# Performance work log

Measured on AMD Instinct MI355X. Metric: run time of the kernel, lower is better.

The kernel has to match this reference:

```python
import jax, jax.numpy as jnp
import numpy as np

B, V, DEMB, H, LAT, L = 16384, 64, 128, 512, 128, 2
PAD, BOS, EOS = 0, 1, 2


def setup_inputs() -> dict:
    key = jax.random.key(0)
    ks = jax.random.split(key, 12)
    s = 0.05  # small init so softmax logits stay well-scaled
    z = jax.random.normal(ks[0], (B, LAT), jnp.float32)
    E = jax.random.normal(ks[1], (V, DEMB), jnp.float32) * s
    E = E.at[PAD].set(0.0)  # padding_idx row is zero
    W_l2h = jax.random.normal(ks[2], (H, LAT), jnp.float32) * s
    b_l2h = jnp.zeros((H,), jnp.float32)
    W_ih0 = jax.random.normal(ks[3], (4 * H, DEMB), jnp.float32) * s
    W_hh0 = jax.random.normal(ks[4], (4 * H, H), jnp.float32) * s
    b_ih0 = jnp.zeros((4 * H,), jnp.float32)
    b_hh0 = jnp.zeros((4 * H,), jnp.float32)
    W_ih1 = jax.random.normal(ks[5], (4 * H, H), jnp.float32) * s
    W_hh1 = jax.random.normal(ks[6], (4 * H, H), jnp.float32) * s
    b_ih1 = jnp.zeros((4 * H,), jnp.float32)
    b_hh1 = jnp.zeros((4 * H,), jnp.float32)
    W_out = jax.random.normal(ks[7], (V, H), jnp.float32) * s
    b_out = jnp.zeros((V,), jnp.float32)
    return {"z": z, "E": E, "W_l2h": W_l2h, "b_l2h": b_l2h,
            "W_ih0": W_ih0, "W_hh0": W_hh0, "b_ih0": b_ih0, "b_hh0": b_hh0,
            "W_ih1": W_ih1, "W_hh1": W_hh1, "b_ih1": b_ih1, "b_hh1": b_hh1,
            "W_out": W_out, "b_out": b_out, "max_len": 100}


def _lstm_cell(x, h, c, Wih, Whh, bih, bhh):
    # torch LSTM gate order: i, f, g, o
    g = x @ Wih.T + bih + h @ Whh.T + bhh  # [B, 4H]
    i, f, gg, o = jnp.split(g, 4, axis=-1)
    c_new = jax.nn.sigmoid(f) * c + jax.nn.sigmoid(i) * jnp.tanh(gg)
    h_new = jax.nn.sigmoid(o) * jnp.tanh(c_new)
    return h_new, c_new


def reference(z, E, W_l2h, b_l2h, W_ih0, W_hh0, b_ih0, b_hh0,
              W_ih1, W_hh1, b_ih1, b_hh1, W_out, b_out, max_len):
    # initial states: c0 = latent2hidden(z) repeated over layers, h0 = 0
    c0 = z @ W_l2h.T + b_l2h                      # [B, H]
    c = jnp.stack([c0, c0])                       # [L, B, H]
    h = jnp.zeros_like(c)
    prev = jnp.full((B,), BOS, jnp.int32)
    is_end = jnp.zeros((B,), bool)
    keys = jax.random.split(jax.random.key(42), max_len)

    def step(carry, k):
        h, c, prev, is_end = carry
        x = E[prev]                               # [B, DEMB]
        h0, c0_ = _lstm_cell(x, h[0], c[0], W_ih0, W_hh0, b_ih0, b_hh0)
        h1, c1_ = _lstm_cell(h0, h[1], c[1], W_ih1, W_hh1, b_ih1, b_hh1)
        logits = h1 @ W_out.T + b_out             # [B, V]
        cur = jax.random.categorical(k, logits)   # same dist as Categorical(softmax(logits))
        is_end = is_end | (cur == EOS)            # mark eos; eos itself becomes pad
        cur = jnp.where(is_end, PAD, cur).astype(jnp.int32)
        return (jnp.stack([h0, h1]), jnp.stack([c0_, c1_]), cur, is_end), cur

    _, samples = jax.lax.scan(step, (h, c, prev, is_end), keys)  # [T, B]
    return samples.T                              # [B, T]
```

## Files before the change

kernel.cpp:

```cpp
#include <hip/hip_runtime.h>
#include <stdint.h>

#define B_    16384
#define V_    64
#define DEMB_ 128
#define H_    512
#define PAD_  0
#define BOS_  1
#define EOS_  2

__device__ __forceinline__ uint32_t rotl32(uint32_t v, int n) {
    return (v << n) | (v >> (32 - n));
}

__device__ __forceinline__ void tf2x32(uint32_t k0, uint32_t k1,
                                       uint32_t x0, uint32_t x1,
                                       uint32_t& o0, uint32_t& o1)
{
    const uint32_t k2 = k0 ^ k1 ^ 0x1BD11BDAu;
    x0 += k0; x1 += k1;
#define TFR(r) { x0 += x1; x1 = rotl32(x1, (r)); x1 ^= x0; }
    TFR(13) TFR(15) TFR(26) TFR(6)
    x0 += k1; x1 += k2 + 1u;
    TFR(17) TFR(29) TFR(16) TFR(24)
    x0 += k2; x1 += k0 + 2u;
    TFR(13) TFR(15) TFR(26) TFR(6)
    x0 += k0; x1 += k1 + 3u;
    TFR(17) TFR(29) TFR(16) TFR(24)
    x0 += k1; x1 += k2 + 4u;
    TFR(13) TFR(15) TFR(26) TFR(6)
    x0 += k2; x1 += k0 + 5u;
#undef TFR
    o0 = x0; o1 = x1;
}

__device__ __forceinline__ float sigm(float x) {
    return 1.0f / (1.0f + expf(-x));
}

__device__ __forceinline__ float4 ld4(const float* p) {
    return *reinterpret_cast<const float4*>(p);
}

__global__ __launch_bounds__(256)
void init_state(const float* __restrict__ z, const float* __restrict__ Wl,
                const float* __restrict__ bl,
                float* __restrict__ C0, float* __restrict__ C1,
                float* __restrict__ H0, float* __restrict__ H1)
{
    __shared__ __align__(16) float As[16][68];
    __shared__ __align__(16) float Bs[16][68];
    const int tid  = threadIdx.x;
    const int b0   = blockIdx.x * 64;
    const int j0   = blockIdx.y * 64;
    const int tx   = tid & 15, ty = tid >> 4;
    const int lrow = tid >> 2, lkq = tid & 3;

    float acc[4][4] = {};

    for (int kt = 0; kt < DEMB_ / 16; ++kt) {
        const int k0 = kt * 16;
        float4 av = ld4(z  + (size_t)(b0 + lrow) * DEMB_ + k0 + lkq * 4);
        float4 bv = ld4(Wl + (size_t)(j0 + lrow) * DEMB_ + k0 + lkq * 4);
        __syncthreads();
        As[lkq*4+0][lrow] = av.x; As[lkq*4+1][lrow] = av.y; As[lkq*4+2][lrow] = av.z; As[lkq*4+3][lrow] = av.w;
        Bs[lkq*4+0][lrow] = bv.x; Bs[lkq*4+1][lrow] = bv.y; Bs[lkq*4+2][lrow] = bv.z; Bs[lkq*4+3][lrow] = bv.w;
        __syncthreads();
#pragma unroll
        for (int kk = 0; kk < 16; ++kk) {
            float4 a4 = ld4(&As[kk][ty*4]);
            float4 b4 = ld4(&Bs[kk][tx*4]);
            float ar[4] = {a4.x, a4.y, a4.z, a4.w};
            float br[4] = {b4.x, b4.y, b4.z, b4.w};
#pragma unroll
            for (int r = 0; r < 4; ++r)
#pragma unroll
                for (int c = 0; c < 4; ++c)
                    acc[r][c] = fmaf(ar[r], br[c], acc[r][c]);
        }
    }

#pragma unroll
    for (int r = 0; r < 4; ++r) {
        const int b = b0 + ty * 4 + r;
        const int j = j0 + tx * 4;
        float4 cv = {acc[r][0] + bl[j+0], acc[r][1] + bl[j+1],
                     acc[r][2] + bl[j+2], acc[r][3] + bl[j+3]};
        float4 zz = {0.f, 0.f, 0.f, 0.f};
        *reinterpret_cast<float4*>(C0 + (size_t)b * H_ + j) = cv;
        *reinterpret_cast<float4*>(C1 + (size_t)b * H_ + j) = cv;
        *reinterpret_cast<float4*>(H0 + (size_t)b * H_ + j) = zz;
        *reinterpret_cast<float4*>(H1 + (size_t)b * H_ + j) = zz;
    }
}

__global__ __launch_bounds__(256)
void init_tokens(int* __restrict__ prevtok, int* __restrict__ isend)
{
    int i = blockIdx.x * 256 + threadIdx.x;
    if (i < B_) { prevtok[i] = BOS_; isend[i] = 0; }
}

template<int KX, bool GATHER>
__global__ __launch_bounds__(256, 2)
void lstm_layer(const float* __restrict__ Asrc,
                const int*   __restrict__ prevtok,
                const float* __restrict__ Hrec,
                const float* __restrict__ Wih,
                const float* __restrict__ Whh,
                const float* __restrict__ bih,
                const float* __restrict__ bhh,
                float* __restrict__ Cst,
                float* __restrict__ Hout)
{
    __shared__ __align__(16) float As[2][16][132];
    __shared__ __align__(16) float Bs[2][4][16][68];
    __shared__ int rowtok[128];

    const int tid  = threadIdx.x;
    const int bid  = blockIdx.x;
    const int b0   = (bid >> 3) * 128;
    const int j0   = (bid & 7) * 64;
    const int tx   = tid & 15;
    const int ty   = tid >> 4;
    const int srow = tid >> 1;
    const int sk   = (tid & 1) * 8;

    if (GATHER) {
        if (tid < 128) rowtok[tid] = prevtok[b0 + tid];
        __syncthreads();
    }

    const int grow0 = srow, grow1 = srow + 128;
    const int g0 = grow0 >> 6, u0 = grow0 & 63;
    const int g1 = grow1 >> 6, u1 = grow1 & 63;

    const float* arowA = GATHER ? (Asrc + (size_t)rowtok[srow] * DEMB_)
                                : (Asrc + (size_t)(b0 + srow) * KX);
    const float* arowH = Hrec + (size_t)(b0 + srow) * H_;
    const float* browA0 = Wih + (size_t)(g0 * H_ + j0 + u0) * KX;
    const float* browA1 = Wih + (size_t)(g1 * H_ + j0 + u1) * KX;
    const float* browH0 = Whh + (size_t)(g0 * H_ + j0 + u0) * H_;
    const float* browH1 = Whh + (size_t)(g1 * H_ + j0 + u1) * H_;

    const int NT = (KX + H_) / 16;

    float4 av[2], bv[4];

    auto load_tile = [&](int kt) {
        const int k0 = kt * 16;
        if (k0 < KX) {
            av[0] = ld4(arowA + k0 + sk);
            av[1] = ld4(arowA + k0 + sk + 4);
            bv[0] = ld4(browA0 + k0 + sk);
            bv[1] = ld4(browA0 + k0 + sk + 4);
            bv[2] = ld4(browA1 + k0 + sk);
            bv[3] = ld4(browA1 + k0 + sk + 4);
        } else {
            const int kh = k0 - KX;
            av[0] = ld4(arowH + kh + sk);
            av[1] = ld4(arowH + kh + sk + 4);
            bv[0] = ld4(browH0 + kh + sk);
            bv[1] = ld4(browH0 + kh + sk + 4);
            bv[2] = ld4(browH1 + kh + sk);
            bv[3] = ld4(browH1 + kh + sk + 4);
        }
    };

    auto write_tile = [&](int p) {
        float a0[4] = {av[0].x, av[0].y, av[0].z, av[0].w};
        float a1[4] = {av[1].x, av[1].y, av[1].z, av[1].w};
#pragma unroll
        for (int i = 0; i < 4; ++i) {
            As[p][sk + i][srow]     = a0[i];
            As[p][sk + 4 + i][srow] = a1[i];
        }
        float b0r[4] = {bv[0].x, bv[0].y, bv[0].z, bv[0].w};
        float b1r[4] = {bv[1].x, bv[1].y, bv[1].z, bv[1].w};
        float b2r[4] = {bv[2].x, bv[2].y, bv[2].z, bv[2].w};
        float b3r[4] = {bv[3].x, bv[3].y, bv[3].z, bv[3].w};
#pragma unroll
        for (int i = 0; i < 4; ++i) {
            Bs[p][g0][sk + i][u0]     = b0r[i];
            Bs[p][g0][sk + 4 + i][u0] = b1r[i];
            Bs[p][g1][sk + i][u1]     = b2r[i];
            Bs[p][g1][sk + 4 + i][u1] = b3r[i];
        }
    };

    load_tile(0);
    write_tile(0);
    load_tile(1);
    __syncthreads();

    float acc[4][8][4] = {};

    for (int kt = 0; kt < NT; ++kt) {
        const int cur = kt & 1;
        if (kt + 1 < NT) {
            write_tile(cur ^ 1);
            if (kt + 2 < NT) load_tile(kt + 2);
        }
#pragma unroll 4
        for (int kk = 0; kk < 16; ++kk) {
            float4 a40 = ld4(&As[cur][kk][ty*8]);
            float4 a41 = ld4(&As[cur][kk][ty*8+4]);
            float ar[8] = {a40.x, a40.y, a40.z, a40.w, a41.x, a41.y, a41.z, a41.w};
#pragma unroll
            for (int g = 0; g < 4; ++g) {
                float4 b4 = ld4(&Bs[cur][g][kk][tx*4]);
                float br[4] = {b4.x, b4.y, b4.z, b4.w};
#pragma unroll
                for (int r = 0; r < 8; ++r)
#pragma unroll
                    for (int c = 0; c < 4; ++c)
                        acc[g][r][c] = fmaf(ar[r], br[c], acc[g][r][c]);
            }
        }
        __syncthreads();
    }

    const int j = j0 + tx * 4;
    float4 bi0 = ld4(bih + 0*H_ + j), bi1 = ld4(bih + 1*H_ + j);
    float4 bi2 = ld4(bih + 2*H_ + j), bi3 = ld4(bih + 3*H_ + j);
    float4 bh0 = ld4(bhh + 0*H_ + j), bh1 = ld4(bhh + 1*H_ + j);
    float4 bh2 = ld4(bhh + 2*H_ + j), bh3 = ld4(bhh + 3*H_ + j);
    float bi[4][4] = {{bi0.x,bi0.y,bi0.z,bi0.w},{bi1.x,bi1.y,bi1.z,bi1.w},
                      {bi2.x,bi2.y,bi2.z,bi2.w},{bi3.x,bi3.y,bi3.z,bi3.w}};
    float bh[4][4] = {{bh0.x,bh0.y,bh0.z,bh0.w},{bh1.x,bh1.y,bh1.z,bh1.w},
                      {bh2.x,bh2.y,bh2.z,bh2.w},{bh3.x,bh3.y,bh3.z,bh3.w}};

#pragma unroll
    for (int r = 0; r < 8; ++r) {
        const int b = b0 + ty * 8 + r;
        float4 c4 = ld4(Cst + (size_t)b * H_ + j);
        float cold[4] = {c4.x, c4.y, c4.z, c4.w};
        float cn[4], hn[4];
#pragma unroll
        for (int c = 0; c < 4; ++c) {
            float gi = acc[0][r][c] + bi[0][c] + bh[0][c];
            float gf = acc[1][r][c] + bi[1][c] + bh[1][c];
            float gg = acc[2][r][c] + bi[2][c] + bh[2][c];
            float go = acc[3][r][c] + bi[3][c] + bh[3][c];
            float si = sigm(gi), sf = sigm(gf), so = sigm(go);
            float tg = tanhf(gg);
            float cc = __fadd_rn(__fmul_rn(sf, cold[c]), __fmul_rn(si, tg));
            cn[c] = cc;
            hn[c] = __fmul_rn(so, tanhf(cc));
        }
        float4 co = {cn[0], cn[1], cn[2], cn[3]};
        float4 ho = {hn[0], hn[1], hn[2], hn[3]};
        *reinterpret_cast<float4*>(Cst  + (size_t)b * H_ + j) = co;
        *reinterpret_cast<float4*>(Hout + (size_t)b * H_ + j) = ho;
    }
}

__global__ __launch_bounds__(256)
void sample_step(const float* __restrict__ H1src, const float* __restrict__ Wout,
                 const float* __restrict__ bout,
                 int* __restrict__ prevtok, int* __restrict__ isend,
                 int* __restrict__ out, int t, int T)
{
    __shared__ __align__(16) float As[16][68];
    __shared__ __align__(16) float Bs[16][68];
    __shared__ float LG[64][65];

    const int tid  = threadIdx.x;
    const int b0   = blockIdx.x * 64;
    const int tx   = tid & 15, ty = tid >> 4;
    const int lrow = tid >> 2, lkq = tid & 3;

    float acc[4][4] = {};

    for (int kt = 0; kt < H_ / 16; ++kt) {
        const int k0 = kt * 16;
        float4 av = ld4(H1src + (size_t)(b0 + lrow) * H_ + k0 + lkq * 4);
        float4 bv = ld4(Wout  + (size_t)lrow * H_ + k0 + lkq * 4);
        __syncthreads();
        As[lkq*4+0][lrow] = av.x; As[lkq*4+1][lrow] = av.y; As[lkq*4+2][lrow] = av.z; As[lkq*4+3][lrow] = av.w;
        Bs[lkq*4+0][lrow] = bv.x; Bs[lkq*4+1][lrow] = bv.y; Bs[lkq*4+2][lrow] = bv.z; Bs[lkq*4+3][lrow] = bv.w;
        __syncthreads();
#pragma unroll
        for (int kk = 0; kk < 16; ++kk) {
            float4 a4 = ld4(&As[kk][ty*4]);
            float4 b4 = ld4(&Bs[kk][tx*4]);
            float ar[4] = {a4.x, a4.y, a4.z, a4.w};
            float br[4] = {b4.x, b4.y, b4.z, b4.w};
#pragma unroll
            for (int r = 0; r < 4; ++r)
#pragma unroll
                for (int c = 0; c < 4; ++c)
                    acc[r][c] = fmaf(ar[r], br[c], acc[r][c]);
        }
    }

#pragma unroll
    for (int r = 0; r < 4; ++r)
#pragma unroll
        for (int c = 0; c < 4; ++c)
            LG[ty*4 + r][tx*4 + c] = acc[r][c] + bout[tx*4 + c];
    __syncthreads();

    const int wv = tid >> 6, lane = tid & 63;
    uint32_t kt0, kt1;
    tf2x32(0u, 42u, 0u, (uint32_t)t, kt0, kt1);

    const float TINY = 1.1754943508222875e-38f;
    for (int rr = 0; rr < 16; ++rr) {
        const int r = wv * 16 + rr;
        const int b = b0 + r;
        float lg = LG[r][lane];
        uint32_t r0, r1;
        tf2x32(kt0, kt1, 0u, (uint32_t)(b * V_ + lane), r0, r1);
        uint32_t bits = r0 ^ r1;
        float f = __uint_as_float((bits >> 9) | 0x3f800000u) - 1.0f;
        float u = fmaxf(TINY, __fadd_rn(f, TINY));
        float g = -logf(-logf(u));
        float val = __fadd_rn(g, lg);
        int idx = lane;
#pragma unroll
        for (int off = 32; off > 0; off >>= 1) {
            float ov = __shfl_xor(val, off, 64);
            int   oi = __shfl_xor(idx, off, 64);
            if (ov > val || (ov == val && oi < idx)) { val = ov; idx = oi; }
        }
        if (lane == 0) {
            int cur = idx;
            int e   = isend[b];
            int en  = e | (cur == EOS_);
            int tok = en ? PAD_ : cur;
            isend[b]   = en;
            prevtok[b] = tok;
            out[(size_t)b * T + t] = tok;
        }
    }
}

extern "C" void kernel_launch(void* const* d_in, const int* in_sizes, int n_in,
                              void* d_out, int out_size, void* d_ws, size_t ws_size,
                              hipStream_t stream)
{
    (void)in_sizes; (void)n_in; (void)ws_size;
    const float* z    = (const float*)d_in[0];
    const float* E    = (const float*)d_in[1];
    const float* Wl2h = (const float*)d_in[2];
    const float* bl2h = (const float*)d_in[3];
    const float* Wih0 = (const float*)d_in[4];
    const float* Whh0 = (const float*)d_in[5];
    const float* bih0 = (const float*)d_in[6];
    const float* bhh0 = (const float*)d_in[7];
    const float* Wih1 = (const float*)d_in[8];
    const float* Whh1 = (const float*)d_in[9];
    const float* bih1 = (const float*)d_in[10];
    const float* bhh1 = (const float*)d_in[11];
    const float* Wout = (const float*)d_in[12];
    const float* bout = (const float*)d_in[13];
    int* out = (int*)d_out;
    const int T = out_size / B_;

    char* w = (char*)d_ws;
    const size_t S = (size_t)B_ * H_ * sizeof(float);
    float* C0  = (float*)(w + 0 * S);
    float* C1  = (float*)(w + 1 * S);
    float* H0A = (float*)(w + 2 * S);
    float* H0B = (float*)(w + 3 * S);
    float* H1A = (float*)(w + 4 * S);
    float* H1B = (float*)(w + 5 * S);
    int* prevtok = (int*)(w + 6 * S);
    int* isend   = (int*)(w + 6 * S + (size_t)B_ * sizeof(int));

    dim3 blk(256);
    init_state<<<dim3(B_/64, H_/64), blk, 0, stream>>>(z, Wl2h, bl2h, C0, C1, H0A, H1A);
    init_tokens<<<dim3(B_/256), blk, 0, stream>>>(prevtok, isend);

    float *h0c = H0A, *h0n = H0B, *h1c = H1A, *h1n = H1B;
    for (int t = 0; t < T; ++t) {
        lstm_layer<DEMB_, true><<<dim3((B_/128) * 8), blk, 0, stream>>>(
            E, prevtok, h0c, Wih0, Whh0, bih0, bhh0, C0, h0n);
        lstm_layer<H_, false><<<dim3((B_/128) * 8), blk, 0, stream>>>(
            h0n, nullptr, h1c, Wih1, Whh1, bih1, bhh1, C1, h1n);
        sample_step<<<dim3(B_/64), blk, 0, stream>>>(
            h1n, Wout, bout, prevtok, isend, out, t, T);
        float* tmp;
        tmp = h0c; h0c = h0n; h0n = tmp;
        tmp = h1c; h1c = h1n; h1n = tmp;
    }
}
```

Before: 132.1 ms.

## Precompute embedding-times-Wih0 table and pipeline smaller-tile sampling GEMM

Because the layer-0 input is always an embedding row, E·Wih0ᵀ is precomputed once into a 64×2048 table. The layer-0 kernel then seeds its accumulators from that table by token id instead of running the K=128 input GEMM every step, which removes about 20% of layer-0 FLOPs. Separately, the sampling kernel now uses 32-row tiles with double-buffered shared memory and launch bounds of 2, giving more blocks and overlapping loads with compute. Pre-adding x·W in a different order may change float rounding slightly.

```diff
diff --git a/kernel.cpp b/kernel.cpp
--- a/kernel.cpp
+++ b/kernel.cpp
@@ -41,6 +41,9 @@
 __device__ __forceinline__ float4 ld4(const float* p) {
     return *reinterpret_cast<const float4*>(p);
 }
+__device__ __forceinline__ float2 ld2(const float* p) {
+    return *reinterpret_cast<const float2*>(p);
+}
 
 __global__ __launch_bounds__(256)
 void init_state(const float* __restrict__ z, const float* __restrict__ Wl,
@@ -101,10 +104,26 @@
     if (i < B_) { prevtok[i] = BOS_; isend[i] = 0; }
 }
 
-template<int KX, bool GATHER>
+__global__ __launch_bounds__(256)
+void build_xw0(const float* __restrict__ E, const float* __restrict__ Wih0,
+               float* __restrict__ XW0)
+{
+    const int idx = blockIdx.x * 256 + threadIdx.x;
+    const int v = idx >> 11;
+    const int n = idx & 2047;
+    const float* e = E + (size_t)v * DEMB_;
+    const float* w = Wih0 + (size_t)n * DEMB_;
+    float acc = 0.f;
+    for (int k = 0; k < DEMB_; ++k)
+        acc = fmaf(e[k], w[k], acc);
+    XW0[(size_t)v * 2048 + n] = acc;
+}
+
+template<int KX, bool XW>
 __global__ __launch_bounds__(256, 2)
 void lstm_layer(const float* __restrict__ Asrc,
                 const int*   __restrict__ prevtok,
+                const float* __restrict__ XW0,
                 const float* __restrict__ Hrec,
                 const float* __restrict__ Wih,
                 const float* __restrict__ Whh,
@@ -126,7 +145,7 @@
     const int srow = tid >> 1;
     const int sk   = (tid & 1) * 8;
 
-    if (GATHER) {
+    if (XW) {
         if (tid < 128) rowtok[tid] = prevtok[b0 + tid];
         __syncthreads();
     }
@@ -135,11 +154,10 @@
     const int g0 = grow0 >> 6, u0 = grow0 & 63;
     const int g1 = grow1 >> 6, u1 = grow1 & 63;
 
-    const float* arowA = GATHER ? (Asrc + (size_t)rowtok[srow] * DEMB_)
-                                : (Asrc + (size_t)(b0 + srow) * KX);
+    const float* arowA = (KX > 0) ? (Asrc + (size_t)(b0 + srow) * KX) : nullptr;
     const float* arowH = Hrec + (size_t)(b0 + srow) * H_;
-    const float* browA0 = Wih + (size_t)(g0 * H_ + j0 + u0) * KX;
-    const float* browA1 = Wih + (size_t)(g1 * H_ + j0 + u1) * KX;
+    const float* browA0 = (KX > 0) ? (Wih + (size_t)(g0 * H_ + j0 + u0) * KX) : nullptr;
+    const float* browA1 = (KX > 0) ? (Wih + (size_t)(g1 * H_ + j0 + u1) * KX) : nullptr;
     const float* browH0 = Whh + (size_t)(g0 * H_ + j0 + u0) * H_;
     const float* browH1 = Whh + (size_t)(g1 * H_ + j0 + u1) * H_;
 
@@ -149,7 +167,7 @@
 
     auto load_tile = [&](int kt) {
         const int k0 = kt * 16;
-        if (k0 < KX) {
+        if (KX > 0 && k0 < KX) {
             av[0] = ld4(arowA + k0 + sk);
             av[1] = ld4(arowA + k0 + sk + 4);
             bv[0] = ld4(browA0 + k0 + sk);
@@ -188,12 +206,33 @@
         }
     };
 
+    float acc[4][8][4];
+    if (XW) {
+#pragma unroll
+        for (int r = 0; r < 8; ++r) {
+            const int tok = rowtok[ty * 8 + r];
+            const float* xr = XW0 + (size_t)tok * 2048 + j0 + tx * 4;
+#pragma unroll
+            for (int g = 0; g < 4; ++g) {
+                float4 x4 = ld4(xr + g * H_);
+                acc[g][r][0] = x4.x; acc[g][r][1] = x4.y;
+                acc[g][r][2] = x4.z; acc[g][r][3] = x4.w;
+            }
+        }
+    } else {
+#pragma unroll
+        for (int g = 0; g < 4; ++g)
+#pragma unroll
+            for (int r = 0; r < 8; ++r)
+#pragma unroll
+                for (int c = 0; c < 4; ++c)
+                    acc[g][r][c] = 0.f;
+    }
+
     load_tile(0);
     write_tile(0);
     load_tile(1);
     __syncthreads();
-
-    float acc[4][8][4] = {};
 
     for (int kt = 0; kt < NT; ++kt) {
         const int cur = kt & 1;
@@ -255,50 +294,74 @@
     }
 }
 
-__global__ __launch_bounds__(256)
+__global__ __launch_bounds__(256, 2)
 void sample_step(const float* __restrict__ H1src, const float* __restrict__ Wout,
                  const float* __restrict__ bout,
                  int* __restrict__ prevtok, int* __restrict__ isend,
                  int* __restrict__ out, int t, int T)
 {
-    __shared__ __align__(16) float As[16][68];
-    __shared__ __align__(16) float Bs[16][68];
-    __shared__ float LG[64][65];
+    __shared__ __align__(16) float As[2][16][36];
+    __shared__ __align__(16) float Bs[2][16][68];
+    __shared__ float LG[32][65];
 
     const int tid  = threadIdx.x;
-    const int b0   = blockIdx.x * 64;
+    const int b0   = blockIdx.x * 32;
     const int tx   = tid & 15, ty = tid >> 4;
-    const int lrow = tid >> 2, lkq = tid & 3;
-
-    float acc[4][4] = {};
-
-    for (int kt = 0; kt < H_ / 16; ++kt) {
+    const int arow = tid >> 3, ak = (tid & 7) * 2;
+    const int brow = tid >> 2, bk = (tid & 3) * 4;
+
+    const float* aptr = H1src + (size_t)(b0 + arow) * H_;
+    const float* bptr = Wout  + (size_t)brow * H_;
+
+    float2 av;
+    float4 bv;
+    auto load_tile = [&](int kt) {
         const int k0 = kt * 16;
-        float4 av = ld4(H1src + (size_t)(b0 + lrow) * H_ + k0 + lkq * 4);
-        float4 bv = ld4(Wout  + (size_t)lrow * H_ + k0 + lkq * 4);
-        __syncthreads();
-        As[lkq*4+0][lrow] = av.x; As[lkq*4+1][lrow] = av.y; As[lkq*4+2][lrow] = av.z; As[lkq*4+3][lrow] = av.w;
-        Bs[lkq*4+0][lrow] = bv.x; Bs[lkq*4+1][lrow] = bv.y; Bs[lkq*4+2][lrow] = bv.z; Bs[lkq*4+3][lrow] = bv.w;
-        __syncthreads();
-#pragma unroll
+        av = ld2(aptr + k0 + ak);
+        bv = ld4(bptr + k0 + bk);
+    };
+    auto write_tile = [&](int p) {
+        As[p][ak + 0][arow] = av.x;
+        As[p][ak + 1][arow] = av.y;
+        float br[4] = {bv.x, bv.y, bv.z, bv.w};
+#pragma unroll
+        for (int i = 0; i < 4; ++i) Bs[p][bk + i][brow] = br[i];
+    };
+
+    float acc[2][4] = {};
+
+    load_tile(0);
+    write_tile(0);
+    load_tile(1);
+    __syncthreads();
+
+    const int NT = H_ / 16;
+    for (int kt = 0; kt < NT; ++kt) {
+        const int cur = kt & 1;
+        if (kt + 1 < NT) {
+            write_tile(cur ^ 1);
+            if (kt + 2 < NT) load_tile(kt + 2);
+        }
+#pragma unroll 4
         for (int kk = 0; kk < 16; ++kk) {
-            float4 a4 = ld4(&As[kk][ty*4]);
-            float4 b4 = ld4(&Bs[kk][tx*4]);
-            float ar[4] = {a4.x, a4.y, a4.z, a4.w};
+            float2 a2 = ld2(&As[cur][kk][ty*2]);
+            float4 b4 = ld4(&Bs[cur][kk][tx*4]);
+            float ar[2] = {a2.x, a2.y};
             float br[4] = {b4.x, b4.y, b4.z, b4.w};
 #pragma unroll
-            for (int r = 0; r < 4; ++r)
+            for (int r = 0; r < 2; ++r)
 #pragma unroll
                 for (int c = 0; c < 4; ++c)
                     acc[r][c] = fmaf(ar[r], br[c], acc[r][c]);
         }
-    }
-
-#pragma unroll
-    for (int r = 0; r < 4; ++r)
+        __syncthreads();
+    }
+
+#pragma unroll
+    for (int r = 0; r < 2; ++r)
 #pragma unroll
         for (int c = 0; c < 4; ++c)
-            LG[ty*4 + r][tx*4 + c] = acc[r][c] + bout[tx*4 + c];
+            LG[ty*2 + r][tx*4 + c] = acc[r][c] + bout[tx*4 + c];
     __syncthreads();
 
     const int wv = tid >> 6, lane = tid & 63;
@@ -306,8 +369,8 @@
     tf2x32(0u, 42u, 0u, (uint32_t)t, kt0, kt1);
 
     const float TINY = 1.1754943508222875e-38f;
-    for (int rr = 0; rr < 16; ++rr) {
-        const int r = wv * 16 + rr;
+    for (int rr = 0; rr < 8; ++rr) {
+        const int r = wv * 8 + rr;
         const int b = b0 + r;
         float lg = LG[r][lane];
         uint32_t r0, r1;
@@ -368,18 +431,20 @@
     float* H1B = (float*)(w + 5 * S);
     int* prevtok = (int*)(w + 6 * S);
     int* isend   = (int*)(w + 6 * S + (size_t)B_ * sizeof(int));
+    float* XW0   = (float*)(w + 6 * S + 2 * (size_t)B_ * sizeof(int));
 
     dim3 blk(256);
     init_state<<<dim3(B_/64, H_/64), blk, 0, stream>>>(z, Wl2h, bl2h, C0, C1, H0A, H1A);
     init_tokens<<<dim3(B_/256), blk, 0, stream>>>(prevtok, isend);
+    build_xw0<<<dim3(64 * 2048 / 256), blk, 0, stream>>>(E, Wih0, XW0);
 
     float *h0c = H0A, *h0n = H0B, *h1c = H1A, *h1n = H1B;
     for (int t = 0; t < T; ++t) {
-        lstm_layer<DEMB_, true><<<dim3((B_/128) * 8), blk, 0, stream>>>(
-            E, prevtok, h0c, Wih0, Whh0, bih0, bhh0, C0, h0n);
+        lstm_layer<0, true><<<dim3((B_/128) * 8), blk, 0, stream>>>(
+            nullptr, prevtok, XW0, h0c, nullptr, Whh0, bih0, bhh0, C0, h0n);
         lstm_layer<H_, false><<<dim3((B_/128) * 8), blk, 0, stream>>>(
-            h0n, nullptr, h1c, Wih1, Whh1, bih1, bhh1, C1, h1n);
-        sample_step<<<dim3(B_/64), blk, 0, stream>>>(
+            h0n, nullptr, nullptr, h1c, Wih1, Whh1, bih1, bhh1, C1, h1n);
+        sample_step<<<dim3(B_/32), blk, 0, stream>>>(
             h1n, Wout, bout, prevtok, isend, out, t, T);
         float* tmp;
         tmp = h0c; h0c = h0n; h0n = tmp;
```

Result: faster. 128.7 ms, median of 2 (-2.5%).
